# Optimization experiments

Hardware: AMD Instinct MI355X
Metric: run time of the kernel (lower is better)

Reference implementation:

```python
import jax, jax.numpy as jnp
import numpy as np

N, E, B, L = 32768, 524288, 64, 4
ESM, S, V, EH = 1280, 128, 16, 64
N_RBF = 16
CENTERS = jnp.linspace(0.0, 12.0, N_RBF)
GAMMA = 1.0 / ((12.0 / N_RBF) ** 2 + 1e-8)
LN_EPS = 1e-5


def setup_inputs() -> dict:
    key = jax.random.key(0)
    ks = iter(jax.random.split(key, 80))
    def w(shape, scale=0.02):
        return (jax.random.normal(next(ks), shape) * scale).astype(jnp.float32)
    def zeros(shape):
        return jnp.zeros(shape, jnp.float32)
    def ones(shape):
        return jnp.ones(shape, jnp.float32)
    inp = {}
    inp['x_esm'] = jax.random.normal(next(ks), (N, ESM), jnp.float32)
    inp['x_reschem'] = jax.random.normal(next(ks), (N, 6), jnp.float32)
    inp['x_role'] = jax.random.uniform(next(ks), (N, 2), jnp.float32)
    inp['x_dist_raw'] = jax.random.uniform(next(ks), (N, 4), jnp.float32) * 12.0
    inp['x_misc'] = jax.random.normal(next(ks), (N, 3), jnp.float32)
    inp['x_vec'] = jax.random.normal(next(ks), (N, 1, 3), jnp.float32)
    inp['pos'] = jax.random.normal(next(ks), (N, 3), jnp.float32) * 10.0
    inp['edge_dist_raw'] = jax.random.uniform(next(ks), (E, 2), jnp.float32) * 12.0
    # node scalar encoder
    inp['ne_esm_w'] = w((ESM, 128)); inp['ne_esm_b'] = zeros((128,))
    inp['ne_esm_ln_g'] = ones((128,)); inp['ne_esm_ln_b'] = zeros((128,))
    in_dim = 128 + 6 + 2 + 3 + 4 * N_RBF  # 203
    inp['ne_out_w'] = w((in_dim, S)); inp['ne_out_b'] = zeros((S,))
    inp['ne_out_ln_g'] = ones((S,)); inp['ne_out_ln_b'] = zeros((S,))
    # edge scalar encoder
    inp['ee_w'] = w((2 * N_RBF, EH)); inp['ee_b'] = zeros((EH,))
    inp['ee_ln_g'] = ones((EH,)); inp['ee_ln_b'] = zeros((EH,))
    inp['init_vec_w'] = w((1, V))
    # stacked per-layer params
    msi = 2 * S + EH + 1 + (2 * V + 1)  # scalar_mlp in for message gvp = 354
    usi = 2 * S + 2 * V                 # = 288
    inp['msg_s_w1'] = w((L, msi, S)); inp['msg_s_b1'] = zeros((L, S))
    inp['msg_s_w2'] = w((L, S, S)); inp['msg_s_b2'] = zeros((L, S))
    inp['msg_v_w'] = w((L, 2 * V + 1, V))
    inp['msg_g_w'] = w((L, S, V)); inp['msg_g_b'] = zeros((L, V))
    inp['upd_s_w1'] = w((L, usi, S)); inp['upd_s_b1'] = zeros((L, S))
    inp['upd_s_w2'] = w((L, S, S)); inp['upd_s_b2'] = zeros((L, S))
    inp['upd_v_w'] = w((L, 2 * V, V))
    inp['upd_g_w'] = w((L, S, V)); inp['upd_g_b'] = zeros((L, V))
    inp['ln_g'] = ones((L, S)); inp['ln_b'] = zeros((L, S))
    # heads
    inp['hm_w1'] = w((2 * S, S)); inp['hm_b1'] = zeros((S,))
    inp['hm_w2'] = w((S, 8)); inp['hm_b2'] = zeros((8,))
    inp['he_w1'] = w((2 * S, S)); inp['he_b1'] = zeros((S,))
    inp['he_w2'] = w((S, 7)); inp['he_b2'] = zeros((7,))
    inp['edge_index'] = jax.random.randint(next(ks), (2, E), 0, N, jnp.int32)
    inp['batch'] = jnp.sort(jax.random.randint(next(ks), (N,), 0, B, jnp.int32))
    return inp


def _ln(x, g, b):
    mu = x.mean(-1, keepdims=True)
    var = ((x - mu) ** 2).mean(-1, keepdims=True)
    return (x - mu) * jax.lax.rsqrt(var + LN_EPS) * g + b


def _rbf(d):
    # d [..., K] -> [..., K, N_RBF]
    return jnp.exp(-GAMMA * (d[..., None] - CENTERS) ** 2)


def _vnorm(v):
    # v [N, C, 3] -> [N, C]
    return jnp.sqrt(jnp.clip((v * v).sum(-1), 1e-8))


def _gvp(s, v, sw1, sb1, sw2, sb2, vw, gw, gb):
    s_cat = jnp.concatenate([s, _vnorm(v)], -1)
    h = jax.nn.silu(s_cat @ sw1 + sb1)
    s_out = h @ sw2 + sb2
    v_proj = jnp.einsum('nci,cv->nvi', v, vw)
    gate = jax.nn.sigmoid(s_out @ gw + gb)[..., None]
    return s_out, v_proj * gate


def _forward(x_esm, x_reschem, x_role, x_dist_raw, x_misc, x_vec, pos, edge_dist_raw,
             ne_esm_w, ne_esm_b, ne_esm_ln_g, ne_esm_ln_b, ne_out_w, ne_out_b,
             ne_out_ln_g, ne_out_ln_b, ee_w, ee_b, ee_ln_g, ee_ln_b, init_vec_w,
             msg_s_w1, msg_s_b1, msg_s_w2, msg_s_b2, msg_v_w, msg_g_w, msg_g_b,
             upd_s_w1, upd_s_b1, upd_s_w2, upd_s_b2, upd_v_w, upd_g_w, upd_g_b,
             ln_g, ln_b, hm_w1, hm_b1, hm_w2, hm_b2, he_w1, he_b1, he_w2, he_b2,
             edge_index, batch):
    n = x_esm.shape[0]
    # node scalar encoder (dropout = identity at eval)
    esm = jax.nn.silu(_ln(x_esm @ ne_esm_w + ne_esm_b, ne_esm_ln_g, ne_esm_ln_b))
    d_rbf = _rbf(x_dist_raw).reshape(n, -1)  # [N, 64]
    xcat = jnp.concatenate([esm, x_reschem, x_role, x_misc, d_rbf], -1)
    s = jax.nn.silu(_ln(xcat @ ne_out_w + ne_out_b, ne_out_ln_g, ne_out_ln_b))
    # init vector channels [N, V, 3]
    v = jnp.einsum('nci,cv->nvi', x_vec, init_vec_w)
    # edge scalar encoder
    e_rbf = _rbf(edge_dist_raw).reshape(edge_dist_raw.shape[0], -1)  # [E, 32]
    edge_s = jax.nn.silu(_ln(e_rbf @ ee_w + ee_b, ee_ln_g, ee_ln_b))
    # edge vectors [E, 1, 3]
    src, dst = edge_index[0], edge_index[1]
    rel = pos[dst] - pos[src]
    rel = rel / jnp.sqrt(jnp.clip((rel * rel).sum(-1, keepdims=True), 1e-8))
    edge_v = rel[:, None, :]
    edge_len = _vnorm(edge_v)  # [E, 1]
    for l in range(L):
        m_s_in = jnp.concatenate([s[src], s[dst], edge_s, edge_len], -1)
        m_v_in = jnp.concatenate([v[src], v[dst], edge_v], 1)
        m_s, m_v = _gvp(m_s_in, m_v_in, msg_s_w1[l], msg_s_b1[l], msg_s_w2[l],
                        msg_s_b2[l], msg_v_w[l], msg_g_w[l], msg_g_b[l])
        agg_s = jax.ops.segment_sum(m_s, dst, num_segments=n)
        agg_v = jax.ops.segment_sum(m_v, dst, num_segments=n)
        u_s_in = jnp.concatenate([s, agg_s], -1)
        u_v_in = jnp.concatenate([v, agg_v], 1)
        ds, dv = _gvp(u_s_in, u_v_in, upd_s_w1[l], upd_s_b1[l], upd_s_w2[l],
                      upd_s_b2[l], upd_v_w[l], upd_g_w[l], upd_g_b[l])
        s = _ln(s + ds, ln_g[l], ln_b[l])
        v = v + dv
    # graph pooling
    sums = jax.ops.segment_sum(s, batch, num_segments=B)
    cnts = jax.ops.segment_sum(jnp.ones((n, 1), s.dtype), batch, num_segments=B)
    pooled_mean = sums / jnp.clip(cnts, 1.0)
    pooled_max = jax.ops.segment_max(s, batch, num_segments=B)
    pooled_max = jnp.where(jnp.isfinite(pooled_max), pooled_max, 0.0)
    embed = jnp.concatenate([pooled_mean, pooled_max], -1)
    logits_metal = jax.nn.silu(embed @ hm_w1 + hm_b1) @ hm_w2 + hm_b2
    logits_ec = jax.nn.silu(embed @ he_w1 + he_b1) @ he_w2 + he_b2
    return logits_metal, logits_ec, embed


def reference(x_esm, x_reschem, x_role, x_dist_raw, x_misc, x_vec, pos, edge_dist_raw,
              ne_esm_w, ne_esm_b, ne_esm_ln_g, ne_esm_ln_b, ne_out_w, ne_out_b,
              ne_out_ln_g, ne_out_ln_b, ee_w, ee_b, ee_ln_g, ee_ln_b, init_vec_w,
              msg_s_w1, msg_s_b1, msg_s_w2, msg_s_b2, msg_v_w, msg_g_w, msg_g_b,
              upd_s_w1, upd_s_b1, upd_s_w2, upd_s_b2, upd_v_w, upd_g_w, upd_g_b,
              ln_g, ln_b, hm_w1, hm_b1, hm_w2, hm_b2, he_w1, he_b1, he_w2, he_b2,
              edge_index, batch):
    return _forward(x_esm, x_reschem, x_role, x_dist_raw, x_misc, x_vec, pos,
                    edge_dist_raw, ne_esm_w, ne_esm_b, ne_esm_ln_g, ne_esm_ln_b,
                    ne_out_w, ne_out_b, ne_out_ln_g, ne_out_ln_b, ee_w, ee_b,
                    ee_ln_g, ee_ln_b, init_vec_w, msg_s_w1, msg_s_b1, msg_s_w2,
                    msg_s_b2, msg_v_w, msg_g_w, msg_g_b, upd_s_w1, upd_s_b1,
                    upd_s_w2, upd_s_b2, upd_v_w, upd_g_w, upd_g_b, ln_g, ln_b,
                    hm_w1, hm_b1, hm_w2, hm_b2, he_w1, he_b1, he_w2, he_b2,
                    edge_index, batch)
```

## Files before the change

### kernel.cpp

```cpp
#include <hip/hip_runtime.h>
#include <hip/hip_bf16.h>
#include <cstddef>

constexpr int kN = 32768;
constexpr int kE = 524288;
constexpr int kB = 64;
constexpr int kL = 4;
constexpr float kGamma = (float)(1.0 / (0.5625 + 1e-8));
constexpr float kLnEps = 1e-5f;

#define DI __device__ __forceinline__

typedef __attribute__((ext_vector_type(8))) short bf16x8;
typedef __attribute__((ext_vector_type(4))) short s16x4;
typedef __attribute__((ext_vector_type(4))) float f32x4;
#define MFMA16(a, b, c) __builtin_amdgcn_mfma_f32_16x16x32_bf16(a, b, c, 0, 0, 0)

DI float siluf(float x) { return x / (1.f + __expf(-x)); }
DI float sigmf(float x) { return 1.f / (1.f + __expf(-x)); }
DI unsigned short f2bf(float x) {
  __hip_bfloat16 b = __float2bfloat16(x);
  return *(unsigned short*)&b;
}
DI float b2f(unsigned short u) {
  union { unsigned i; float f; } c; c.i = ((unsigned)u) << 16; return c.f;
}
DI bf16x8 ldA(const float* p) {
  const float4 a = *(const float4*)p;
  const float4 b = *(const float4*)(p + 4);
  bf16x8 r;
  r[0] = (short)f2bf(a.x); r[1] = (short)f2bf(a.y);
  r[2] = (short)f2bf(a.z); r[3] = (short)f2bf(a.w);
  r[4] = (short)f2bf(b.x); r[5] = (short)f2bf(b.y);
  r[6] = (short)f2bf(b.z); r[7] = (short)f2bf(b.w);
  return r;
}

__global__ void k_btA(const float* src, unsigned short* dst, int K) {
  int idx = blockIdx.x * 256 + threadIdx.x;
  if (idx >= K * 128) return;
  int c = idx & 127, k = idx >> 7;
  dst[c * K + k] = f2bf(src[(size_t)k * 128 + c]);
}

__global__ void k_bt1(const float* w, unsigned short* dst) {
  int idx = blockIdx.x * 256 + threadIdx.x;
  int c = idx & 127, k = idx >> 7;
  dst[c * 224 + k] = f2bf(k < 203 ? w[(size_t)k * 128 + c] : 0.f);
}

__global__ void k_btPQ(const float* w1, unsigned short* dst) {
  int idx = blockIdx.x * 256 + threadIdx.x;
  int cc = idx / 160, k = idx - cc * 160;
  int c = cc & 127, half = cc >> 7;
  float v = 0.f;
  if (k < 128) v = w1[(size_t)(half * 128 + k) * 128 + c];
  else if (k < 144) v = w1[(size_t)(321 + half * 16 + (k - 128)) * 128 + c];
  dst[idx] = f2bf(v);
}

__global__ void k_w2gw(const float* w2, const float* gw, const float* b2, const float* gb,
                       float* out) {
  int idx = blockIdx.x * 256 + threadIdx.x;
  if (idx < 2048) {
    int k = idx >> 4, t = idx & 15;
    float a = 0.f;
    for (int j = 0; j < 128; j++) a += w2[(size_t)k * 128 + j] * gw[j * 16 + t];
    out[idx] = a;
  } else if (idx < 2064) {
    int t = idx - 2048;
    float a = gb[t];
    for (int j = 0; j < 128; j++) a += b2[j] * gw[j * 16 + t];
    out[idx] = a;
  }
}

__global__ void k_xrest(const float* resch, const float* role, const float* misc,
                        const float* dist, float* xr) {
  int idx = blockIdx.x * 256 + threadIdx.x;
  int r = idx / 96, c = idx - r * 96;
  float v = 0.f;
  if (c < 6) v = resch[r * 6 + c];
  else if (c < 8) v = role[r * 2 + c - 6];
  else if (c < 11) v = misc[r * 3 + c - 8];
  else if (c < 75) {
    int j = c - 11;
    float d = dist[r * 4 + (j >> 4)];
    float t = d - 0.8f * (float)(j & 15);
    v = __expf(-kGamma * t * t);
  }
  xr[idx] = v;
}

struct G2 {
  const float* A1; const float* A2; const float* A3;
  const unsigned short* BT;
  float* out;
  unsigned short* obfP; unsigned short* obfQ;
  const float* bias; const float* lng; const float* lnb;
};

template <int MODE>
__global__ __launch_bounds__(256) void k_gemm2(G2 p) {
  constexpr int K = MODE == 0 ? 1280 : MODE == 1 ? 224 : MODE == 2 ? 160 : 288;
  constexpr int NS = K / 32;
  constexpr int NTC = (MODE == 2) ? 16 : 8;
  const int tid = threadIdx.x, lane = tid & 63, wv = tid >> 6;
  const int g4 = lane >> 4, lc = lane & 15;
  const int r = blockIdx.x * 64 + wv * 16 + lc;
  const f32x4 z = {0.f, 0.f, 0.f, 0.f};
  f32x4 acc[NTC];
#pragma unroll
  for (int nt = 0; nt < NTC; nt++) acc[nt] = z;

  if constexpr (MODE == 0) {
#pragma unroll 4
    for (int ks = 0; ks < NS; ks++) {
      const int k = ks * 32 + g4 * 8;
      const bf16x8 af = ldA(p.A1 + (size_t)r * 1280 + k);
#pragma unroll
      for (int nt = 0; nt < NTC; nt++)
        acc[nt] = MFMA16(af, *(const bf16x8*)&p.BT[(lc + 16 * nt) * K + k], acc[nt]);
    }
  } else {
#pragma unroll
    for (int ks = 0; ks < NS; ks++) {
      const int k = ks * 32 + g4 * 8;
      const float* ap;
      if constexpr (MODE == 1)
        ap = (k < 128) ? p.A1 + (size_t)r * 128 + k : p.A2 + (size_t)r * 96 + (k - 128);
      else if constexpr (MODE == 2)
        ap = (k < 128) ? p.A1 + (size_t)r * 128 + k : p.A2 + (size_t)r * 32 + (k - 128);
      else
        ap = (k < 128) ? p.A1 + (size_t)r * 128 + k
           : (k < 256) ? p.A2 + (size_t)r * 128 + (k - 128)
                       : p.A3 + (size_t)r * 32 + (k - 256);
      const bf16x8 af = ldA(ap);
#pragma unroll
      for (int nt = 0; nt < NTC; nt++)
        acc[nt] = MFMA16(af, *(const bf16x8*)&p.BT[(lc + 16 * nt) * K + k], acc[nt]);
    }
  }

  const int row0 = blockIdx.x * 64 + wv * 16 + g4 * 4;
  if constexpr (MODE == 0 || MODE == 1) {
    float bias8[8], g8[8], b8[8];
#pragma unroll
    for (int nt = 0; nt < 8; nt++) {
      int c = lc + 16 * nt;
      bias8[nt] = p.bias[c]; g8[nt] = p.lng[c]; b8[nt] = p.lnb[c];
    }
    float rsum[4] = {0.f, 0.f, 0.f, 0.f}, rsq[4] = {0.f, 0.f, 0.f, 0.f};
#pragma unroll
    for (int nt = 0; nt < 8; nt++)
#pragma unroll
      for (int i = 0; i < 4; i++) {
        float x = acc[nt][i] + bias8[nt];
        acc[nt][i] = x; rsum[i] += x; rsq[i] += x * x;
      }
#pragma unroll
    for (int m = 1; m < 16; m <<= 1)
#pragma unroll
      for (int i = 0; i < 4; i++) {
        rsum[i] += __shfl_xor(rsum[i], m);
        rsq[i] += __shfl_xor(rsq[i], m);
      }
#pragma unroll
    for (int i = 0; i < 4; i++) {
      float mu = rsum[i] * (1.f / 128.f);
      float rs = rsqrtf(rsq[i] * (1.f / 128.f) - mu * mu + kLnEps);
#pragma unroll
      for (int nt = 0; nt < 8; nt++) {
        float y = (acc[nt][i] - mu) * rs * g8[nt] + b8[nt];
        p.out[(size_t)(row0 + i) * 128 + lc + 16 * nt] = siluf(y);
      }
    }
  } else if constexpr (MODE == 2) {
#pragma unroll
    for (int i = 0; i < 4; i++) {
      bf16x8 po, qo;
#pragma unroll
      for (int nt = 0; nt < 8; nt++) {
        po[nt] = (short)f2bf(acc[nt][i]);
        qo[nt] = (short)f2bf(acc[nt + 8][i] + p.bias[lc + 16 * nt]);
      }
      *(bf16x8*)&p.obfP[(size_t)(row0 + i) * 128 + lc * 8] = po;
      *(bf16x8*)&p.obfQ[(size_t)(row0 + i) * 128 + lc * 8] = qo;
    }
  } else {
#pragma unroll
    for (int nt = 0; nt < 8; nt++) {
      float bv = p.bias[lc + 16 * nt];
#pragma unroll
      for (int i = 0; i < 4; i++)
        p.out[(size_t)(row0 + i) * 128 + lc + 16 * nt] = siluf(acc[nt][i] + bv);
    }
  }
}

__global__ void k_v0(const float* xv, const float* ivw, float* v) {
  int idx = blockIdx.x * 256 + threadIdx.x;
  int n = idx / 48, f = idx % 48, t = f / 3, i = f - t * 3;
  v[idx] = xv[n * 3 + i] * ivw[t];
}

__global__ void k_vn(const float* v, float* vn) {
  int idx = blockIdx.x * 256 + threadIdx.x;
  int n = idx >> 5, t = idx & 31;
  float val = 0.f;
  if (t < 16) {
    const float* b = &v[(size_t)n * 48 + t * 3];
    val = sqrtf(fmaxf(b[0] * b[0] + b[1] * b[1] + b[2] * b[2], 1e-8f));
  }
  vn[idx] = val;
}

__global__ void k_vab(const float* v, const float* vw,
                      unsigned short* VAb, unsigned short* VBb) {
  int idx = blockIdx.x * 256 + threadIdx.x;
  int n = idx >> 4, t = idx & 15;
  float a0 = 0.f, a1 = 0.f, a2 = 0.f, b0 = 0.f, b1 = 0.f, b2 = 0.f;
#pragma unroll
  for (int c = 0; c < 16; c++) {
    float wa = vw[c * 16 + t], wb = vw[(16 + c) * 16 + t];
    float x0 = v[(size_t)n * 48 + c * 3 + 0];
    float x1 = v[(size_t)n * 48 + c * 3 + 1];
    float x2 = v[(size_t)n * 48 + c * 3 + 2];
    a0 += x0 * wa; a1 += x1 * wa; a2 += x2 * wa;
    b0 += x0 * wb; b1 += x1 * wb; b2 += x2 * wb;
  }
  s16x4 A, Bv;
  A[0] = (short)f2bf(a0); A[1] = (short)f2bf(a1); A[2] = (short)f2bf(a2); A[3] = 0;
  Bv[0] = (short)f2bf(b0); Bv[1] = (short)f2bf(b1); Bv[2] = (short)f2bf(b2); Bv[3] = 0;
  *(s16x4*)&VAb[(size_t)n * 64 + t * 4] = A;
  *(s16x4*)&VBb[(size_t)n * 64 + t * 4] = Bv;
}

__global__ void k_hist(const int* ei, int* cnt) {
  int e = blockIdx.x * 256 + threadIdx.x;
  atomicAdd(&cnt[ei[kE + e]], 1);
}

__global__ __launch_bounds__(1024) void k_scan(const int* cnt, int* rowstart, int* cursor) {
  __shared__ int part[1024];
  const int t = threadIdx.x;
  const int base = t * 32;
  int loc[32];
  int s = 0;
#pragma unroll
  for (int i = 0; i < 32; i++) { loc[i] = cnt[base + i]; s += loc[i]; }
  part[t] = s;
  __syncthreads();
  for (int off = 1; off < 1024; off <<= 1) {
    int val = (t >= off) ? part[t - off] : 0;
    __syncthreads();
    part[t] += val;
    __syncthreads();
  }
  int run = (t == 0) ? 0 : part[t - 1];
#pragma unroll
  for (int i = 0; i < 32; i++) {
    rowstart[base + i] = run;
    cursor[base + i] = run;
    run += loc[i];
  }
  if (t == 1023) rowstart[kN] = run;
}

__global__ void k_scatter(const int* ei, const float* pos, int* cursor,
                          int* prm, int* srcp, float* relp, float* lenp) {
  int e = blockIdx.x * 256 + threadIdx.x;
  int a = ei[e], b = ei[kE + e];
  int p = atomicAdd(&cursor[b], 1);
  prm[p] = e;
  srcp[p] = a;
  float dx = pos[(size_t)b * 3 + 0] - pos[(size_t)a * 3 + 0];
  float dy = pos[(size_t)b * 3 + 1] - pos[(size_t)a * 3 + 1];
  float dz = pos[(size_t)b * 3 + 2] - pos[(size_t)a * 3 + 2];
  float n2 = dx * dx + dy * dy + dz * dz;
  float inv = 1.f / sqrtf(fmaxf(n2, 1e-8f));
  float rx = dx * inv, ry = dy * inv, rz = dz * inv;
  relp[(size_t)p * 3 + 0] = rx; relp[(size_t)p * 3 + 1] = ry; relp[(size_t)p * 3 + 2] = rz;
  lenp[p] = sqrtf(fmaxf(rx * rx + ry * ry + rz * rz, 1e-8f));
}

__global__ __launch_bounds__(256) void k_enc_mfma(
    const int* __restrict__ prm, const float* __restrict__ edr,
    const float* __restrict__ eew, const float* __restrict__ eeb,
    const float* __restrict__ lg, const float* __restrict__ lb,
    __hip_bfloat16* __restrict__ enc) {
  __shared__ unsigned short eewT[64 * 32];
  const int tid = threadIdx.x;
#pragma unroll
  for (int i = 0; i < 8; i++) {
    int idx = tid + i * 256;
    int col = idx >> 5, k = idx & 31;
    eewT[col * 32 + k] = f2bf(eew[k * 64 + col]);
  }
  __syncthreads();

  const int lane = tid & 63, wv = tid >> 6;
  const int g4 = lane >> 4, lc = lane & 15;
  const int e0 = blockIdx.x * 64 + wv * 16;

  const int e = prm[e0 + lc];
  const float d = edr[(size_t)e * 2 + (g4 >> 1)];
  const float c0 = 0.8f * (float)((g4 & 1) * 8);
  bf16x8 af;
#pragma unroll
  for (int j = 0; j < 8; j++) {
    float t = d - (c0 + 0.8f * (float)j);
    af[j] = (short)f2bf(__expf(-kGamma * t * t));
  }
  const f32x4 z = {0.f, 0.f, 0.f, 0.f};
  f32x4 acc[4];
#pragma unroll
  for (int ct = 0; ct < 4; ct++)
    acc[ct] = MFMA16(af, *(const bf16x8*)&eewT[(ct * 16 + lc) * 32 + g4 * 8], z);

  float bias4[4], g4v[4], b4[4];
#pragma unroll
  for (int ct = 0; ct < 4; ct++) {
    int col = ct * 16 + lc;
    bias4[ct] = eeb[col]; g4v[ct] = lg[col]; b4[ct] = lb[col];
  }
  float rsum[4] = {0.f, 0.f, 0.f, 0.f}, rsq[4] = {0.f, 0.f, 0.f, 0.f};
#pragma unroll
  for (int ct = 0; ct < 4; ct++)
#pragma unroll
    for (int i = 0; i < 4; i++) {
      float x = acc[ct][i] + bias4[ct];
      acc[ct][i] = x; rsum[i] += x; rsq[i] += x * x;
    }
#pragma unroll
  for (int m = 1; m < 16; m <<= 1)
#pragma unroll
    for (int i = 0; i < 4; i++) {
      rsum[i] += __shfl_xor(rsum[i], m);
      rsq[i] += __shfl_xor(rsq[i], m);
    }
#pragma unroll
  for (int i = 0; i < 4; i++) {
    float mu = rsum[i] * (1.f / 64.f);
    float rs = rsqrtf(rsq[i] * (1.f / 64.f) - mu * mu + kLnEps);
    const size_t row = (size_t)(e0 + g4 * 4 + i);
#pragma unroll
    for (int ct = 0; ct < 4; ct++) {
      float y = (acc[ct][i] - mu) * rs * g4v[ct] + b4[ct];
      enc[row * 64 + ct * 16 + lc] = __float2bfloat16(siluf(y));
    }
  }
}

struct __align__(16) EMS2 {
  unsigned short we1T[128 * 72];
  unsigned short w2T[128 * 136];
  unsigned short w2gwT[16 * 72];
  unsigned short h[8][16 * 72];
  float wlen[128];
  float b2[128];
  float gb[16];
  float vw32[16];
};

__global__ __launch_bounds__(512, 4) void k_node_msg(
    const unsigned short* __restrict__ Pb, const unsigned short* __restrict__ Qb,
    const unsigned short* __restrict__ VAb, const unsigned short* __restrict__ VBb,
    const __hip_bfloat16* __restrict__ enc_, const float* __restrict__ relp,
    const float* __restrict__ lenp, const int* __restrict__ srcp,
    const int* __restrict__ rowstart, const float* __restrict__ vglob,
    const float* __restrict__ w1, const float* __restrict__ w2g,
    const float* __restrict__ b2g, const float* __restrict__ w2gw,
    const float* __restrict__ vwg,
    float* __restrict__ aggs, float* __restrict__ aggv, float* __restrict__ vnu) {
  __shared__ EMS2 sm;
  const int tid = threadIdx.x;
  const unsigned short* enc = (const unsigned short*)enc_;

#pragma unroll
  for (int i = 0; i < 16; i++) {
    int idx = tid + i * 512; int k = idx >> 7, n = idx & 127;
    sm.we1T[n * 72 + k] = f2bf(w1[(size_t)(256 + k) * 128 + n]);
  }
#pragma unroll
  for (int i = 0; i < 32; i++) {
    int idx = tid + i * 512; int k = idx >> 7, n = idx & 127;
    sm.w2T[n * 136 + k] = f2bf(w2g[(size_t)k * 128 + n]);
  }
#pragma unroll
  for (int i = 0; i < 4; i++) {
    int idx = tid + i * 512; int k = idx >> 4, t = idx & 15;
    sm.w2gwT[t * 72 + k] = f2bf(w2gw[k * 16 + t]);
  }
  if (tid < 128) { sm.wlen[tid] = w1[320 * 128 + tid] + w1[353 * 128 + tid]; sm.b2[tid] = b2g[tid]; }
  if (tid < 16) { sm.gb[tid] = w2gw[2048 + tid]; sm.vw32[tid] = vwg[512 + tid]; }
  __syncthreads();

  const int lane = tid & 63, wv = tid >> 6;
  const int g4 = lane >> 4;
  const int lc = lane & 15;
  unsigned short* hrow = &sm.h[wv][0];

  float wlenR[8], b2R[8];
#pragma unroll
  for (int nt = 0; nt < 8; nt++) { wlenR[nt] = sm.wlen[lc + 16 * nt]; b2R[nt] = sm.b2[lc + 16 * nt]; }
  const float gbR = sm.gb[lc];
  const float vwR = sm.vw32[lc];
  const f32x4 z = {0.f, 0.f, 0.f, 0.f};

  for (int n = blockIdx.x * 8 + wv; n < kN; n += gridDim.x * 8) {
    const int r0 = rowstart[n], r1 = rowstart[n + 1];
    float qR[8], vbR[3];
    {
      const bf16x8 qv = *(const bf16x8*)&Qb[(size_t)n * 128 + lc * 8];
#pragma unroll
      for (int nt = 0; nt < 8; nt++) qR[nt] = b2f((unsigned short)qv[nt]);
      const s16x4 vbv = *(const s16x4*)&VBb[(size_t)n * 64 + lc * 4];
#pragma unroll
      for (int j = 0; j < 3; j++) vbR[j] = b2f((unsigned short)vbv[j]);
    }
    float colsum[8];
#pragma unroll
    for (int nt = 0; nt < 8; nt++) colsum[nt] = 0.f;
    float av0 = 0.f, av1 = 0.f, av2 = 0.f;

    for (int base = r0; base < r1; base += 16) {
      int nv = r1 - base; if (nv > 16) nv = 16;

      int pa = base + lc; if (pa >= kE) pa = kE - 1;
      const bf16x8 a0 = *(const bf16x8*)&enc[(size_t)pa * 64 + g4 * 8];
      const bf16x8 a1 = *(const bf16x8*)&enc[(size_t)pa * 64 + 32 + g4 * 8];
      f32x4 acc[8];
#pragma unroll
      for (int nt = 0; nt < 8; nt++) {
        acc[nt] = MFMA16(a0, *(const bf16x8*)&sm.we1T[(lc + 16 * nt) * 72 + g4 * 8], z);
        acc[nt] = MFMA16(a1, *(const bf16x8*)&sm.we1T[(lc + 16 * nt) * 72 + 32 + g4 * 8], acc[nt]);
      }

      int sn[4], pr[4]; float le[4];
#pragma unroll
      for (int i = 0; i < 4; i++) {
        int p = base + g4 * 4 + i; if (p >= kE) p = kE - 1;
        pr[i] = p; sn[i] = srcp[p]; le[i] = lenp[p];
      }
#pragma unroll
      for (int i = 0; i < 4; i++) {
        const bf16x8 pbv = *(const bf16x8*)&Pb[(size_t)sn[i] * 128 + lc * 8];
#pragma unroll
        for (int nt = 0; nt < 8; nt++)
          acc[nt][i] += b2f((unsigned short)pbv[nt]) + qR[nt] + le[i] * wlenR[nt];
      }

      f32x4 m[8]; f32x4 gac;
#pragma unroll
      for (int i = 0; i < 4; i++)
#pragma unroll
        for (int nt = 0; nt < 4; nt++)
          hrow[(g4 * 4 + i) * 72 + lc + 16 * nt] = f2bf(siluf(acc[nt][i]));
      {
        const bf16x8 aB0 = *(const bf16x8*)&hrow[lc * 72 + g4 * 8];
        const bf16x8 aB1 = *(const bf16x8*)&hrow[lc * 72 + 32 + g4 * 8];
#pragma unroll
        for (int nt = 0; nt < 8; nt++) {
          m[nt] = MFMA16(aB0, *(const bf16x8*)&sm.w2T[(lc + 16 * nt) * 136 + g4 * 8], z);
          m[nt] = MFMA16(aB1, *(const bf16x8*)&sm.w2T[(lc + 16 * nt) * 136 + 32 + g4 * 8], m[nt]);
        }
        gac = MFMA16(aB0, *(const bf16x8*)&sm.w2gwT[lc * 72 + g4 * 8], z);
        gac = MFMA16(aB1, *(const bf16x8*)&sm.w2gwT[lc * 72 + 32 + g4 * 8], gac);
      }
#pragma unroll
      for (int i = 0; i < 4; i++)
#pragma unroll
        for (int nt = 4; nt < 8; nt++)
          hrow[(g4 * 4 + i) * 72 + lc + 16 * (nt - 4)] = f2bf(siluf(acc[nt][i]));
      {
        const bf16x8 aB2 = *(const bf16x8*)&hrow[lc * 72 + g4 * 8];
        const bf16x8 aB3 = *(const bf16x8*)&hrow[lc * 72 + 32 + g4 * 8];
#pragma unroll
        for (int nt = 0; nt < 8; nt++) {
          m[nt] = MFMA16(aB2, *(const bf16x8*)&sm.w2T[(lc + 16 * nt) * 136 + 64 + g4 * 8], m[nt]);
          m[nt] = MFMA16(aB3, *(const bf16x8*)&sm.w2T[(lc + 16 * nt) * 136 + 96 + g4 * 8], m[nt]);
        }
        gac = MFMA16(aB2, *(const bf16x8*)&sm.w2gwT[lc * 72 + 64 + g4 * 8], gac);
        gac = MFMA16(aB3, *(const bf16x8*)&sm.w2gwT[lc * 72 + 96 + g4 * 8], gac);
      }
#pragma unroll
      for (int nt = 0; nt < 8; nt++) {
#pragma unroll
        for (int i = 0; i < 4; i++) m[nt][i] += b2R[nt];
      }

#pragma unroll
      for (int i = 0; i < 4; i++) {
        const int row = g4 * 4 + i;
        if (row < nv) {
#pragma unroll
          for (int nt = 0; nt < 8; nt++) colsum[nt] += m[nt][i];
          float g = sigmf(gac[i] + gbR);
          const s16x4 vav = *(const s16x4*)&VAb[(size_t)sn[i] * 64 + lc * 4];
          const float* rp = &relp[(size_t)pr[i] * 3];
          av0 += g * (b2f((unsigned short)vav[0]) + vbR[0] + rp[0] * vwR);
          av1 += g * (b2f((unsigned short)vav[1]) + vbR[1] + rp[1] * vwR);
          av2 += g * (b2f((unsigned short)vav[2]) + vbR[2] + rp[2] * vwR);
        }
      }
    }

#pragma unroll
    for (int nt = 0; nt < 8; nt++) {
      colsum[nt] += __shfl_xor(colsum[nt], 16);
      colsum[nt] += __shfl_xor(colsum[nt], 32);
    }
    av0 += __shfl_xor(av0, 16); av0 += __shfl_xor(av0, 32);
    av1 += __shfl_xor(av1, 16); av1 += __shfl_xor(av1, 32);
    av2 += __shfl_xor(av2, 16); av2 += __shfl_xor(av2, 32);

    if (g4 == 0) {
#pragma unroll
      for (int nt = 0; nt < 8; nt++) aggs[(size_t)n * 128 + lc + 16 * nt] = colsum[nt];
      aggv[(size_t)n * 48 + lc * 3 + 0] = av0;
      aggv[(size_t)n * 48 + lc * 3 + 1] = av1;
      aggv[(size_t)n * 48 + lc * 3 + 2] = av2;
      vnu[(size_t)n * 32 + 16 + lc] = sqrtf(fmaxf(av0 * av0 + av1 * av1 + av2 * av2, 1e-8f));
    } else if (g4 == 1) {
      float x0 = vglob[(size_t)n * 48 + lc * 3 + 0];
      float x1 = vglob[(size_t)n * 48 + lc * 3 + 1];
      float x2 = vglob[(size_t)n * 48 + lc * 3 + 2];
      vnu[(size_t)n * 32 + lc] = sqrtf(fmaxf(x0 * x0 + x1 * x1 + x2 * x2, 1e-8f));
    }
  }
}

__global__ __launch_bounds__(256) void k_upd2(
    const float* __restrict__ hupd, const unsigned short* __restrict__ BuT,
    const float* __restrict__ b2,
    const float* __restrict__ ugw, const float* __restrict__ ugb, const float* __restrict__ uvw,
    const float* __restrict__ aggv, const float* __restrict__ lng, const float* __restrict__ lnb,
    float* __restrict__ s, float* __restrict__ v, float* __restrict__ vnout) {
  __shared__ __align__(16) float dsb[64 * 129];
  __shared__ float smu[64], srs[64];
  __shared__ float uvwS[512];
  const int tid = threadIdx.x;
  const int bm = blockIdx.x * 64;
  const int lane = tid & 63, wv = tid >> 6;
  const int g4 = lane >> 4, lc = lane & 15;
  uvwS[tid] = uvw[tid]; uvwS[tid + 256] = uvw[tid + 256];
  const f32x4 z = {0.f, 0.f, 0.f, 0.f};
  const int r = bm + wv * 16 + lc;
  f32x4 acc[8];
#pragma unroll
  for (int nt = 0; nt < 8; nt++) acc[nt] = z;

#pragma unroll
  for (int ks = 0; ks < 4; ks++) {
    const int k = ks * 32 + g4 * 8;
    const bf16x8 af = ldA(hupd + (size_t)r * 128 + k);
#pragma unroll
    for (int nt = 0; nt < 8; nt++)
      acc[nt] = MFMA16(af, *(const bf16x8*)&BuT[(lc + 16 * nt) * 128 + k], acc[nt]);
  }
#pragma unroll
  for (int nt = 0; nt < 8; nt++) {
    float bv = b2[lc + 16 * nt];
#pragma unroll
    for (int i = 0; i < 4; i++)
      dsb[(wv * 16 + g4 * 4 + i) * 129 + lc + 16 * nt] = acc[nt][i] + bv;
  }
  __syncthreads();

  const int rr = tid >> 2, p = tid & 3;
  const int n = bm + rr;
  float g[4];
#pragma unroll
  for (int j = 0; j < 4; j++) g[j] = ugb[p * 4 + j];
#pragma unroll 8
  for (int k = 0; k < 128; k++) {
    float m = dsb[rr * 129 + k];
    const float4 wg = *(const float4*)&ugw[k * 16 + p * 4];
    g[0] += m * wg.x; g[1] += m * wg.y; g[2] += m * wg.z; g[3] += m * wg.w;
  }
#pragma unroll
  for (int j = 0; j < 4; j++) g[j] = sigmf(g[j]);

  float vnew[12];
#pragma unroll
  for (int i2 = 0; i2 < 3; i2++) {
    float xv[16], xa[16];
#pragma unroll
    for (int c = 0; c < 16; c++) {
      xv[c] = v[(size_t)n * 48 + c * 3 + i2];
      xa[c] = aggv[(size_t)n * 48 + c * 3 + i2];
    }
#pragma unroll
    for (int j = 0; j < 4; j++) {
      int t = p * 4 + j;
      float a = 0.f;
#pragma unroll
      for (int c = 0; c < 16; c++)
        a += xv[c] * uvwS[c * 16 + t] + xa[c] * uvwS[(16 + c) * 16 + t];
      vnew[j * 3 + i2] = xv[t] + a * g[j];
    }
  }
  if (tid < 64) {
    float sm = 0.f, sq = 0.f;
    for (int c = 0; c < 128; c++) {
      float x = s[(size_t)(bm + tid) * 128 + c] + dsb[tid * 129 + c];
      sm += x; sq += x * x;
    }
    float mu = sm * (1.f / 128.f);
    float var = sq * (1.f / 128.f) - mu * mu;
    smu[tid] = mu; srs[tid] = rsqrtf(var + kLnEps);
  }
  __syncthreads();
#pragma unroll
  for (int j = 0; j < 4; j++) {
    float n0 = vnew[j * 3 + 0], n1 = vnew[j * 3 + 1], n2 = vnew[j * 3 + 2];
#pragma unroll
    for (int i2 = 0; i2 < 3; i2++)
      v[(size_t)n * 48 + (p * 4 + j) * 3 + i2] = vnew[j * 3 + i2];
    vnout[(size_t)n * 32 + p * 4 + j] = sqrtf(fmaxf(n0 * n0 + n1 * n1 + n2 * n2, 1e-8f));
    vnout[(size_t)n * 32 + 16 + p * 4 + j] = 0.f;
  }
#pragma unroll 4
  for (int i = 0; i < 32; i++) {
    int idx = tid + i * 256; int rw = idx >> 7, c = idx & 127;
    float x = s[(size_t)(bm + rw) * 128 + c] + dsb[rw * 129 + c];
    float y = (x - smu[rw]) * srs[rw] * lng[c] + lnb[c];
    s[(size_t)(bm + rw) * 128 + c] = y;
  }
}

DI int lbound(const int* b, int nn, int key) {
  int lo = 0, hi = nn;
  while (lo < hi) { int m = (lo + hi) >> 1; if (b[m] < key) lo = m + 1; else hi = m; }
  return lo;
}

__global__ void k_pool(const float* s, const int* batch, float* dout) {
  int g = blockIdx.x, tid = threadIdx.x;
  int lo = lbound(batch, kN, g), hi = lbound(batch, kN, g + 1);
  float sum = 0.f, mx = -3.402823e38f;
  for (int n = lo; n < hi; n++) {
    float x = s[(size_t)n * 128 + tid];
    sum += x; mx = fmaxf(mx, x);
  }
  int cnt = hi - lo;
  float mean = sum / fmaxf((float)cnt, 1.f);
  if (cnt == 0) mx = 0.f;
  dout[960 + g * 256 + tid] = mean;
  dout[960 + g * 256 + 128 + tid] = mx;
}

__global__ void k_heads(const float* hw1, const float* hb1, const float* hw2, const float* hb2,
                        const float* ew1, const float* eb1, const float* ew2, const float* eb2,
                        float* dout) {
  __shared__ float emb[256], h1[256];
  int g = blockIdx.x, tid = threadIdx.x;
  emb[tid] = dout[960 + g * 256 + tid];
  emb[128 + tid] = dout[960 + g * 256 + 128 + tid];
  __syncthreads();
  float am = hb1[tid], ae = eb1[tid];
#pragma unroll 4
  for (int k = 0; k < 256; k++) {
    float e = emb[k];
    am += e * hw1[k * 128 + tid];
    ae += e * ew1[k * 128 + tid];
  }
  h1[tid] = siluf(am); h1[128 + tid] = siluf(ae);
  __syncthreads();
  if (tid < 8) {
    float a = hb2[tid];
    for (int j = 0; j < 128; j++) a += h1[j] * hw2[j * 8 + tid];
    dout[g * 8 + tid] = a;
  } else if (tid >= 64 && tid < 71) {
    int o = tid - 64;
    float a = eb2[o];
    for (int j = 0; j < 128; j++) a += h1[128 + j] * ew2[j * 7 + o];
    dout[512 + g * 7 + o] = a;
  }
}

extern "C" void kernel_launch(void* const* d_in, const int* in_sizes, int n_in,
                              void* d_out, int out_size, void* d_ws, size_t ws_size,
                              hipStream_t stream) {
  (void)in_sizes; (void)n_in; (void)out_size; (void)ws_size;
  const float* x_esm   = (const float*)d_in[0];
  const float* x_resch = (const float*)d_in[1];
  const float* x_role  = (const float*)d_in[2];
  const float* x_dist  = (const float*)d_in[3];
  const float* x_misc  = (const float*)d_in[4];
  const float* x_vec   = (const float*)d_in[5];
  const float* pos     = (const float*)d_in[6];
  const float* edr     = (const float*)d_in[7];
  const float* ne_esm_w = (const float*)d_in[8];
  const float* ne_esm_b = (const float*)d_in[9];
  const float* ne_esm_lg = (const float*)d_in[10];
  const float* ne_esm_lb = (const float*)d_in[11];
  const float* ne_out_w = (const float*)d_in[12];
  const float* ne_out_b = (const float*)d_in[13];
  const float* ne_out_lg = (const float*)d_in[14];
  const float* ne_out_lb = (const float*)d_in[15];
  const float* ee_w = (const float*)d_in[16];
  const float* ee_b = (const float*)d_in[17];
  const float* ee_lg = (const float*)d_in[18];
  const float* ee_lb = (const float*)d_in[19];
  const float* ivw = (const float*)d_in[20];
  const float* msg_w1 = (const float*)d_in[21];
  const float* msg_b1 = (const float*)d_in[22];
  const float* msg_w2 = (const float*)d_in[23];
  const float* msg_b2 = (const float*)d_in[24];
  const float* msg_vw = (const float*)d_in[25];
  const float* msg_gw = (const float*)d_in[26];
  const float* msg_gb = (const float*)d_in[27];
  const float* upd_w1 = (const float*)d_in[28];
  const float* upd_b1 = (const float*)d_in[29];
  const float* upd_w2 = (const float*)d_in[30];
  const float* upd_b2 = (const float*)d_in[31];
  const float* upd_vw = (const float*)d_in[32];
  const float* upd_gw = (const float*)d_in[33];
  const float* upd_gb = (const float*)d_in[34];
  const float* ln_g = (const float*)d_in[35];
  const float* ln_b = (const float*)d_in[36];
  const float* hm_w1 = (const float*)d_in[37];
  const float* hm_b1 = (const float*)d_in[38];
  const float* hm_w2 = (const float*)d_in[39];
  const float* hm_b2 = (const float*)d_in[40];
  const float* he_w1 = (const float*)d_in[41];
  const float* he_b1 = (const float*)d_in[42];
  const float* he_w2 = (const float*)d_in[43];
  const float* he_b2 = (const float*)d_in[44];
  const int* ei = (const int*)d_in[45];
  const int* batch = (const int*)d_in[46];
  float* dout = (float*)d_out;

  size_t off = 0;
  auto alloc = [&](size_t bytes) {
    void* p = (char*)d_ws + off;
    off += (bytes + 255) & ~(size_t)255;
    return p;
  };
  float* s    = (float*)alloc((size_t)kN * 128 * 4);
  float* v    = (float*)alloc((size_t)kN * 48 * 4);
  float* vn   = (float*)alloc((size_t)kN * 32 * 4);
  unsigned short* Pb = (unsigned short*)alloc((size_t)kN * 128 * 2);
  unsigned short* Qb = (unsigned short*)alloc((size_t)kN * 128 * 2);
  unsigned short* VAb = (unsigned short*)alloc((size_t)kN * 64 * 2);
  unsigned short* VBb = (unsigned short*)alloc((size_t)kN * 64 * 2);
  float* aggS = (float*)alloc((size_t)kN * 128 * 4);
  float* aggV = (float*)alloc((size_t)kN * 48 * 4);
  float* vnu  = (float*)alloc((size_t)kN * 32 * 4);
  float* hupd = (float*)alloc((size_t)kN * 128 * 4);
  float* xrest = (float*)alloc((size_t)kN * 96 * 4);
  __hip_bfloat16* enc = (__hip_bfloat16*)alloc((size_t)kE * 64 * 2);
  float* relp = (float*)alloc((size_t)kE * 3 * 4);
  float* lenp = (float*)alloc((size_t)kE * 4);
  int* srcp   = (int*)alloc((size_t)kE * 4);
  int* prm    = (int*)alloc((size_t)kE * 4);
  int* cnt    = (int*)alloc((size_t)kN * 4);
  int* rowstart = (int*)alloc((size_t)(kN + 1) * 4);
  int* cursor = (int*)alloc((size_t)kN * 4);
  unsigned short* B0T = (unsigned short*)alloc((size_t)128 * 1280 * 2);
  unsigned short* B1T = (unsigned short*)alloc((size_t)128 * 224 * 2);
  unsigned short* B23T = (unsigned short*)alloc((size_t)kL * 256 * 160 * 2);
  unsigned short* B4T = (unsigned short*)alloc((size_t)kL * 128 * 288 * 2);
  unsigned short* BuT = (unsigned short*)alloc((size_t)kL * 128 * 128 * 2);
  float* w2gwL = (float*)alloc((size_t)kL * 2064 * 4);
  float* esm = hupd;

  hipMemsetAsync(cnt, 0, (size_t)kN * 4, stream);
  k_hist<<<kE / 256, 256, 0, stream>>>(ei, cnt);
  k_scan<<<1, 1024, 0, stream>>>(cnt, rowstart, cursor);
  k_scatter<<<kE / 256, 256, 0, stream>>>(ei, pos, cursor, prm, srcp, relp, lenp);
  k_enc_mfma<<<kE / 64, 256, 0, stream>>>(prm, edr, ee_w, ee_b, ee_lg, ee_lb, enc);
  k_btA<<<(1280 * 128 + 255) / 256, 256, 0, stream>>>(ne_esm_w, B0T, 1280);
  k_bt1<<<(224 * 128 + 255) / 256, 256, 0, stream>>>(ne_out_w, B1T);
  k_xrest<<<(kN * 96 + 255) / 256, 256, 0, stream>>>(x_resch, x_role, x_misc, x_dist, xrest);
  for (int l = 0; l < kL; l++) {
    k_btPQ<<<(256 * 160 + 255) / 256, 256, 0, stream>>>(msg_w1 + (size_t)l * 354 * 128,
                                                        B23T + (size_t)l * 256 * 160);
    k_btA<<<(288 * 128 + 255) / 256, 256, 0, stream>>>(upd_w1 + (size_t)l * 288 * 128,
                                                       B4T + (size_t)l * 128 * 288, 288);
    k_btA<<<(128 * 128 + 255) / 256, 256, 0, stream>>>(upd_w2 + (size_t)l * 128 * 128,
                                                       BuT + (size_t)l * 128 * 128, 128);
    k_w2gw<<<9, 256, 0, stream>>>(msg_w2 + (size_t)l * 128 * 128, msg_gw + l * 128 * 16,
                                  msg_b2 + l * 128, msg_gb + l * 16, w2gwL + (size_t)l * 2064);
  }

  {
    G2 p{}; p.A1 = x_esm; p.BT = B0T; p.out = esm;
    p.bias = ne_esm_b; p.lng = ne_esm_lg; p.lnb = ne_esm_lb;
    k_gemm2<0><<<kN / 64, 256, 0, stream>>>(p);
  }
  {
    G2 p{}; p.A1 = esm; p.A2 = xrest; p.BT = B1T; p.out = s;
    p.bias = ne_out_b; p.lng = ne_out_lg; p.lnb = ne_out_lb;
    k_gemm2<1><<<kN / 64, 256, 0, stream>>>(p);
  }
  k_v0<<<kN * 48 / 256, 256, 0, stream>>>(x_vec, ivw, v);
  k_vn<<<kN * 32 / 256, 256, 0, stream>>>(v, vn);

  for (int l = 0; l < kL; l++) {
    const float* w1l = msg_w1 + (size_t)l * 354 * 128;
    const float* b1l = msg_b1 + l * 128;
    const float* w2l = msg_w2 + (size_t)l * 128 * 128;
    const float* b2l = msg_b2 + l * 128;
    const float* vwl = msg_vw + l * 33 * 16;
    const float* ub1 = upd_b1 + l * 128;
    const float* ub2 = upd_b2 + l * 128;
    const float* uvwl = upd_vw + l * 32 * 16;
    const float* ugwl = upd_gw + l * 128 * 16;
    const float* ugbl = upd_gb + l * 16;
    const float* lgl = ln_g + l * 128;
    const float* lbl = ln_b + l * 128;

    {
      G2 p{}; p.A1 = s; p.A2 = vn; p.BT = B23T + (size_t)l * 256 * 160;
      p.obfP = Pb; p.obfQ = Qb; p.bias = b1l;
      k_gemm2<2><<<kN / 64, 256, 0, stream>>>(p);
    }
    k_vab<<<kN * 16 / 256, 256, 0, stream>>>(v, vwl, VAb, VBb);
    k_node_msg<<<512, 512, 0, stream>>>(Pb, Qb, VAb, VBb, enc, relp, lenp, srcp,
                                        rowstart, v, w1l, w2l, b2l,
                                        w2gwL + (size_t)l * 2064, vwl,
                                        aggS, aggV, vnu);
    {
      G2 p{}; p.A1 = s; p.A2 = aggS; p.A3 = vnu; p.BT = B4T + (size_t)l * 128 * 288;
      p.out = hupd; p.bias = ub1;
      k_gemm2<4><<<kN / 64, 256, 0, stream>>>(p);
    }
    k_upd2<<<kN / 64, 256, 0, stream>>>(hupd, BuT + (size_t)l * 128 * 128, ub2,
                                        ugwl, ugbl, uvwl, aggV, lgl, lbl, s, v, vn);
  }

  k_pool<<<kB, 128, 0, stream>>>(s, batch, dout);
  k_heads<<<kB, 128, 0, stream>>>(hm_w1, hm_b1, hm_w2, hm_b2,
                                  he_w1, he_b1, he_w2, he_b2, dout);
}
```

Before: 1.747 ms.

## Fold edge-length and Q terms into MFMA, transpose message layout, stage P/Q stores through LDS

Result: slower. 1.857 ms (+6.3%).

```diff
diff --git a/kernel.cpp b/kernel.cpp
--- a/kernel.cpp
+++ b/kernel.cpp
@@ -176,16 +176,34 @@
       }
     }
   } else if constexpr (MODE == 2) {
-#pragma unroll
-    for (int i = 0; i < 4; i++) {
-      bf16x8 po, qo;
-#pragma unroll
-      for (int nt = 0; nt < 8; nt++) {
-        po[nt] = (short)f2bf(acc[nt][i]);
-        qo[nt] = (short)f2bf(acc[nt + 8][i] + p.bias[lc + 16 * nt]);
-      }
-      *(bf16x8*)&p.obfP[(size_t)(row0 + i) * 128 + lc * 8] = po;
-      *(bf16x8*)&p.obfQ[(size_t)(row0 + i) * 128 + lc * 8] = qo;
+    __shared__ unsigned short sb[64 * 136];
+    const int rl = tid >> 2, seg = tid & 3;
+#pragma unroll
+    for (int nt = 0; nt < 8; nt++)
+#pragma unroll
+      for (int i = 0; i < 4; i++)
+        sb[(wv * 16 + g4 * 4 + i) * 136 + lc + 16 * nt] = f2bf(acc[nt][i]);
+    __syncthreads();
+    {
+      size_t gr = (size_t)(blockIdx.x * 64 + rl) * 128 + seg * 32;
+#pragma unroll
+      for (int u = 0; u < 4; u++)
+        *(bf16x8*)&p.obfP[gr + u * 8] = *(const bf16x8*)&sb[rl * 136 + seg * 32 + u * 8];
+    }
+    __syncthreads();
+#pragma unroll
+    for (int nt = 0; nt < 8; nt++) {
+      float bv = p.bias[lc + 16 * nt];
+#pragma unroll
+      for (int i = 0; i < 4; i++)
+        sb[(wv * 16 + g4 * 4 + i) * 136 + lc + 16 * nt] = f2bf(acc[nt + 8][i] + bv);
+    }
+    __syncthreads();
+    {
+      size_t gr = (size_t)(blockIdx.x * 64 + rl) * 128 + seg * 32;
+#pragma unroll
+      for (int u = 0; u < 4; u++)
+        *(bf16x8*)&p.obfQ[gr + u * 8] = *(const bf16x8*)&sb[rl * 136 + seg * 32 + u * 8];
     }
   } else {
 #pragma unroll
@@ -352,12 +370,12 @@
   }
 }
 
-struct __align__(16) EMS2 {
+struct __align__(16) EMS3 {
   unsigned short we1T[128 * 72];
   unsigned short w2T[128 * 136];
   unsigned short w2gwT[16 * 72];
   unsigned short h[8][16 * 72];
-  float wlen[128];
+  unsigned short Aext[8][256];
   float b2[128];
   float gb[16];
   float vw32[16];
@@ -373,7 +391,7 @@
     const float* __restrict__ b2g, const float* __restrict__ w2gw,
     const float* __restrict__ vwg,
     float* __restrict__ aggs, float* __restrict__ aggv, float* __restrict__ vnu) {
-  __shared__ EMS2 sm;
+  __shared__ EMS3 sm;
   const int tid = threadIdx.x;
   const unsigned short* enc = (const unsigned short*)enc_;
 
@@ -392,7 +410,12 @@
     int idx = tid + i * 512; int k = idx >> 4, t = idx & 15;
     sm.w2gwT[t * 72 + k] = f2bf(w2gw[k * 16 + t]);
   }
-  if (tid < 128) { sm.wlen[tid] = w1[320 * 128 + tid] + w1[353 * 128 + tid]; sm.b2[tid] = b2g[tid]; }
+#pragma unroll
+  for (int i = 0; i < 2; i++) {
+    int idx = tid + i * 512; int w = idx >> 7, oc = idx & 127;
+    sm.Aext[w][oc * 2] = f2bf(w1[320 * 128 + oc] + w1[353 * 128 + oc]);
+  }
+  if (tid < 128) sm.b2[tid] = b2g[tid];
   if (tid < 16) { sm.gb[tid] = w2gw[2048 + tid]; sm.vw32[tid] = vwg[512 + tid]; }
   __syncthreads();
 
@@ -400,21 +423,24 @@
   const int g4 = lane >> 4;
   const int lc = lane & 15;
   unsigned short* hrow = &sm.h[wv][0];
-
-  float wlenR[8], b2R[8];
-#pragma unroll
-  for (int nt = 0; nt < 8; nt++) { wlenR[nt] = sm.wlen[lc + 16 * nt]; b2R[nt] = sm.b2[lc + 16 * nt]; }
+  unsigned short* aext = &sm.Aext[wv][0];
+
+  float b2R[8];
+#pragma unroll
+  for (int nt = 0; nt < 8; nt++) b2R[nt] = sm.b2[lc + 16 * nt];
   const float gbR = sm.gb[lc];
   const float vwR = sm.vw32[lc];
   const f32x4 z = {0.f, 0.f, 0.f, 0.f};
 
   for (int n = blockIdx.x * 8 + wv; n < kN; n += gridDim.x * 8) {
     const int r0 = rowstart[n], r1 = rowstart[n + 1];
-    float qR[8], vbR[3];
     {
-      const bf16x8 qv = *(const bf16x8*)&Qb[(size_t)n * 128 + lc * 8];
-#pragma unroll
-      for (int nt = 0; nt < 8; nt++) qR[nt] = b2f((unsigned short)qv[nt]);
+      unsigned qv = *(const unsigned*)&Qb[(size_t)n * 128 + lane * 2];
+      aext[lane * 4 + 1] = (unsigned short)(qv & 0xffffu);
+      aext[lane * 4 + 3] = (unsigned short)(qv >> 16);
+    }
+    float vbR[3];
+    {
       const s16x4 vbv = *(const s16x4*)&VBb[(size_t)n * 64 + lc * 4];
 #pragma unroll
       for (int j = 0; j < 3; j++) vbR[j] = b2f((unsigned short)vbv[j]);
@@ -428,77 +454,69 @@
       int nv = r1 - base; if (nv > 16) nv = 16;
 
       int pa = base + lc; if (pa >= kE) pa = kE - 1;
+      const int psrc = srcp[pa];
+      const float le = lenp[pa];
       const bf16x8 a0 = *(const bf16x8*)&enc[(size_t)pa * 64 + g4 * 8];
       const bf16x8 a1 = *(const bf16x8*)&enc[(size_t)pa * 64 + 32 + g4 * 8];
-      f32x4 acc[8];
-#pragma unroll
-      for (int nt = 0; nt < 8; nt++) {
-        acc[nt] = MFMA16(a0, *(const bf16x8*)&sm.we1T[(lc + 16 * nt) * 72 + g4 * 8], z);
-        acc[nt] = MFMA16(a1, *(const bf16x8*)&sm.we1T[(lc + 16 * nt) * 72 + 32 + g4 * 8], acc[nt]);
-      }
-
-      int sn[4], pr[4]; float le[4];
-#pragma unroll
-      for (int i = 0; i < 4; i++) {
-        int p = base + g4 * 4 + i; if (p >= kE) p = kE - 1;
-        pr[i] = p; sn[i] = srcp[p]; le[i] = lenp[p];
-      }
-#pragma unroll
-      for (int i = 0; i < 4; i++) {
-        const bf16x8 pbv = *(const bf16x8*)&Pb[(size_t)sn[i] * 128 + lc * 8];
-#pragma unroll
-        for (int nt = 0; nt < 8; nt++)
-          acc[nt][i] += b2f((unsigned short)pbv[nt]) + qR[nt] + le[i] * wlenR[nt];
-      }
-
-      f32x4 m[8]; f32x4 gac;
-#pragma unroll
-      for (int i = 0; i < 4; i++)
-#pragma unroll
-        for (int nt = 0; nt < 4; nt++)
-          hrow[(g4 * 4 + i) * 72 + lc + 16 * nt] = f2bf(siluf(acc[nt][i]));
-      {
-        const bf16x8 aB0 = *(const bf16x8*)&hrow[lc * 72 + g4 * 8];
-        const bf16x8 aB1 = *(const bf16x8*)&hrow[lc * 72 + 32 + g4 * 8];
-#pragma unroll
-        for (int nt = 0; nt < 8; nt++) {
-          m[nt] = MFMA16(aB0, *(const bf16x8*)&sm.w2T[(lc + 16 * nt) * 136 + g4 * 8], z);
-          m[nt] = MFMA16(aB1, *(const bf16x8*)&sm.w2T[(lc + 16 * nt) * 136 + 32 + g4 * 8], m[nt]);
+      bf16x8 be = {0, 0, 0, 0, 0, 0, 0, 0};
+      if (g4 == 0) { be[0] = (short)f2bf(le); be[1] = (short)0x3F80; }
+
+      f32x4 m[8];
+#pragma unroll
+      for (int nt = 0; nt < 8; nt++) m[nt] = z;
+      f32x4 gac = z;
+
+#pragma unroll
+      for (int hh = 0; hh < 2; hh++) {
+        f32x4 acc[4];
+#pragma unroll
+        for (int q = 0; q < 4; q++) {
+          const int nt = hh * 4 + q;
+          const bf16x8 wA0 = *(const bf16x8*)&sm.we1T[(nt * 16 + lc) * 72 + g4 * 8];
+          const bf16x8 wA1 = *(const bf16x8*)&sm.we1T[(nt * 16 + lc) * 72 + 32 + g4 * 8];
+          acc[q] = MFMA16(wA0, a0, z);
+          acc[q] = MFMA16(wA1, a1, acc[q]);
+          bf16x8 ax = {0, 0, 0, 0, 0, 0, 0, 0};
+          if (g4 == 0) {
+            unsigned u = *(const unsigned*)&aext[(nt * 16 + lc) * 2];
+            ax[0] = (short)(u & 0xffffu); ax[1] = (short)(u >> 16);
+          }
+          acc[q] = MFMA16(ax, be, acc[q]);
         }
-        gac = MFMA16(aB0, *(const bf16x8*)&sm.w2gwT[lc * 72 + g4 * 8], z);
-        gac = MFMA16(aB1, *(const bf16x8*)&sm.w2gwT[lc * 72 + 32 + g4 * 8], gac);
-      }
-#pragma unroll
-      for (int i = 0; i < 4; i++)
-#pragma unroll
-        for (int nt = 4; nt < 8; nt++)
-          hrow[(g4 * 4 + i) * 72 + lc + 16 * (nt - 4)] = f2bf(siluf(acc[nt][i]));
-      {
-        const bf16x8 aB2 = *(const bf16x8*)&hrow[lc * 72 + g4 * 8];
-        const bf16x8 aB3 = *(const bf16x8*)&hrow[lc * 72 + 32 + g4 * 8];
-#pragma unroll
-        for (int nt = 0; nt < 8; nt++) {
-          m[nt] = MFMA16(aB2, *(const bf16x8*)&sm.w2T[(lc + 16 * nt) * 136 + 64 + g4 * 8], m[nt]);
-          m[nt] = MFMA16(aB3, *(const bf16x8*)&sm.w2T[(lc + 16 * nt) * 136 + 96 + g4 * 8], m[nt]);
+#pragma unroll
+        for (int q = 0; q < 4; q++) {
+          const int nt = hh * 4 + q;
+          const s16x4 pv = *(const s16x4*)&Pb[(size_t)psrc * 128 + nt * 16 + g4 * 4];
+          s16x4 hv;
+#pragma unroll
+          for (int i = 0; i < 4; i++)
+            hv[i] = (short)f2bf(siluf(acc[q][i] + b2f((unsigned short)pv[i])));
+          *(s16x4*)&hrow[lc * 72 + q * 16 + g4 * 4] = hv;
         }
-        gac = MFMA16(aB2, *(const bf16x8*)&sm.w2gwT[lc * 72 + 64 + g4 * 8], gac);
-        gac = MFMA16(aB3, *(const bf16x8*)&sm.w2gwT[lc * 72 + 96 + g4 * 8], gac);
-      }
-#pragma unroll
-      for (int nt = 0; nt < 8; nt++) {
-#pragma unroll
-        for (int i = 0; i < 4; i++) m[nt][i] += b2R[nt];
+        {
+          const bf16x8 aB0 = *(const bf16x8*)&hrow[lc * 72 + g4 * 8];
+          const bf16x8 aB1 = *(const bf16x8*)&hrow[lc * 72 + 32 + g4 * 8];
+#pragma unroll
+          for (int nt2 = 0; nt2 < 8; nt2++) {
+            m[nt2] = MFMA16(aB0, *(const bf16x8*)&sm.w2T[(lc + 16 * nt2) * 136 + hh * 64 + g4 * 8], m[nt2]);
+            m[nt2] = MFMA16(aB1, *(const bf16x8*)&sm.w2T[(lc + 16 * nt2) * 136 + hh * 64 + 32 + g4 * 8], m[nt2]);
+          }
+          gac = MFMA16(aB0, *(const bf16x8*)&sm.w2gwT[lc * 72 + hh * 64 + g4 * 8], gac);
+          gac = MFMA16(aB1, *(const bf16x8*)&sm.w2gwT[lc * 72 + hh * 64 + 32 + g4 * 8], gac);
+        }
       }
 
 #pragma unroll
       for (int i = 0; i < 4; i++) {
         const int row = g4 * 4 + i;
         if (row < nv) {
-#pragma unroll
-          for (int nt = 0; nt < 8; nt++) colsum[nt] += m[nt][i];
+          int p2 = base + row;
+#pragma unroll
+          for (int nt = 0; nt < 8; nt++) colsum[nt] += m[nt][i] + b2R[nt];
           float g = sigmf(gac[i] + gbR);
-          const s16x4 vav = *(const s16x4*)&VAb[(size_t)sn[i] * 64 + lc * 4];
-          const float* rp = &relp[(size_t)pr[i] * 3];
+          const int sn2 = srcp[p2];
+          const s16x4 vav = *(const s16x4*)&VAb[(size_t)sn2 * 64 + lc * 4];
+          const float* rp = &relp[(size_t)p2 * 3];
           av0 += g * (b2f((unsigned short)vav[0]) + vbR[0] + rp[0] * vwR);
           av1 += g * (b2f((unsigned short)vav[1]) + vbR[1] + rp[1] * vwR);
           av2 += g * (b2f((unsigned short)vav[2]) + vbR[2] + rp[2] * vwR);
```

## Fuse update-MLP first GEMM into update kernel via LDS bf16 staging

Applied to the files above, without the earlier changes.

Result: faster. 1.669 ms (-4.5%).

```diff
diff --git a/kernel.cpp b/kernel.cpp
--- a/kernel.cpp
+++ b/kernel.cpp
@@ -102,7 +102,7 @@
 
 template <int MODE>
 __global__ __launch_bounds__(256) void k_gemm2(G2 p) {
-  constexpr int K = MODE == 0 ? 1280 : MODE == 1 ? 224 : MODE == 2 ? 160 : 288;
+  constexpr int K = MODE == 0 ? 1280 : MODE == 1 ? 224 : 160;
   constexpr int NS = K / 32;
   constexpr int NTC = (MODE == 2) ? 16 : 8;
   const int tid = threadIdx.x, lane = tid & 63, wv = tid >> 6;
@@ -129,12 +129,8 @@
       const float* ap;
       if constexpr (MODE == 1)
         ap = (k < 128) ? p.A1 + (size_t)r * 128 + k : p.A2 + (size_t)r * 96 + (k - 128);
-      else if constexpr (MODE == 2)
+      else
         ap = (k < 128) ? p.A1 + (size_t)r * 128 + k : p.A2 + (size_t)r * 32 + (k - 128);
-      else
-        ap = (k < 128) ? p.A1 + (size_t)r * 128 + k
-           : (k < 256) ? p.A2 + (size_t)r * 128 + (k - 128)
-                       : p.A3 + (size_t)r * 32 + (k - 256);
       const bf16x8 af = ldA(ap);
 #pragma unroll
       for (int nt = 0; nt < NTC; nt++)
@@ -175,7 +171,7 @@
         p.out[(size_t)(row0 + i) * 128 + lc + 16 * nt] = siluf(y);
       }
     }
-  } else if constexpr (MODE == 2) {
+  } else {
 #pragma unroll
     for (int i = 0; i < 4; i++) {
       bf16x8 po, qo;
@@ -186,14 +182,6 @@
       }
       *(bf16x8*)&p.obfP[(size_t)(row0 + i) * 128 + lc * 8] = po;
       *(bf16x8*)&p.obfQ[(size_t)(row0 + i) * 128 + lc * 8] = qo;
-    }
-  } else {
-#pragma unroll
-    for (int nt = 0; nt < 8; nt++) {
-      float bv = p.bias[lc + 16 * nt];
-#pragma unroll
-      for (int i = 0; i < 4; i++)
-        p.out[(size_t)(row0 + i) * 128 + lc + 16 * nt] = siluf(acc[nt][i] + bv);
     }
   }
 }
@@ -531,13 +519,16 @@
   }
 }
 
-__global__ __launch_bounds__(256) void k_upd2(
-    const float* __restrict__ hupd, const unsigned short* __restrict__ BuT,
+__global__ __launch_bounds__(256) void k_upd_fused(
+    const float* __restrict__ sA, const float* __restrict__ aggS,
+    const float* __restrict__ vnu, const unsigned short* __restrict__ B4T,
+    const float* __restrict__ ub1, const unsigned short* __restrict__ BuT,
     const float* __restrict__ b2,
     const float* __restrict__ ugw, const float* __restrict__ ugb, const float* __restrict__ uvw,
     const float* __restrict__ aggv, const float* __restrict__ lng, const float* __restrict__ lnb,
     float* __restrict__ s, float* __restrict__ v, float* __restrict__ vnout) {
   __shared__ __align__(16) float dsb[64 * 129];
+  __shared__ __align__(16) unsigned short hb[64 * 136];
   __shared__ float smu[64], srs[64];
   __shared__ float uvwS[512];
   const int tid = threadIdx.x;
@@ -547,24 +538,47 @@
   uvwS[tid] = uvw[tid]; uvwS[tid + 256] = uvw[tid + 256];
   const f32x4 z = {0.f, 0.f, 0.f, 0.f};
   const int r = bm + wv * 16 + lc;
+
   f32x4 acc[8];
 #pragma unroll
   for (int nt = 0; nt < 8; nt++) acc[nt] = z;
-
+#pragma unroll
+  for (int ks = 0; ks < 9; ks++) {
+    const int k = ks * 32 + g4 * 8;
+    const float* ap = (k < 128) ? sA + (size_t)r * 128 + k
+                    : (k < 256) ? aggS + (size_t)r * 128 + (k - 128)
+                                : vnu + (size_t)r * 32 + (k - 256);
+    const bf16x8 af = ldA(ap);
+#pragma unroll
+    for (int nt = 0; nt < 8; nt++)
+      acc[nt] = MFMA16(af, *(const bf16x8*)&B4T[(lc + 16 * nt) * 288 + k], acc[nt]);
+  }
+#pragma unroll
+  for (int nt = 0; nt < 8; nt++) {
+    float bv = ub1[lc + 16 * nt];
+#pragma unroll
+    for (int i = 0; i < 4; i++)
+      hb[(wv * 16 + g4 * 4 + i) * 136 + lc + 16 * nt] = f2bf(siluf(acc[nt][i] + bv));
+  }
+  __syncthreads();
+
+  f32x4 acc2[8];
+#pragma unroll
+  for (int nt = 0; nt < 8; nt++) acc2[nt] = z;
 #pragma unroll
   for (int ks = 0; ks < 4; ks++) {
     const int k = ks * 32 + g4 * 8;
-    const bf16x8 af = ldA(hupd + (size_t)r * 128 + k);
+    const bf16x8 af = *(const bf16x8*)&hb[(wv * 16 + lc) * 136 + k];
 #pragma unroll
     for (int nt = 0; nt < 8; nt++)
-      acc[nt] = MFMA16(af, *(const bf16x8*)&BuT[(lc + 16 * nt) * 128 + k], acc[nt]);
+      acc2[nt] = MFMA16(af, *(const bf16x8*)&BuT[(lc + 16 * nt) * 128 + k], acc2[nt]);
   }
 #pragma unroll
   for (int nt = 0; nt < 8; nt++) {
     float bv = b2[lc + 16 * nt];
 #pragma unroll
     for (int i = 0; i < 4; i++)
-      dsb[(wv * 16 + g4 * 4 + i) * 129 + lc + 16 * nt] = acc[nt][i] + bv;
+      dsb[(wv * 16 + g4 * 4 + i) * 129 + lc + 16 * nt] = acc2[nt][i] + bv;
   }
   __syncthreads();
 
@@ -823,13 +837,10 @@
                                         rowstart, v, w1l, w2l, b2l,
                                         w2gwL + (size_t)l * 2064, vwl,
                                         aggS, aggV, vnu);
-    {
-      G2 p{}; p.A1 = s; p.A2 = aggS; p.A3 = vnu; p.BT = B4T + (size_t)l * 128 * 288;
-      p.out = hupd; p.bias = ub1;
-      k_gemm2<4><<<kN / 64, 256, 0, stream>>>(p);
-    }
-    k_upd2<<<kN / 64, 256, 0, stream>>>(hupd, BuT + (size_t)l * 128 * 128, ub2,
-                                        ugwl, ugbl, uvwl, aggV, lgl, lbl, s, v, vn);
+    k_upd_fused<<<kN / 64, 256, 0, stream>>>(s, aggS, vnu,
+                                             B4T + (size_t)l * 128 * 288, ub1,
+                                             BuT + (size_t)l * 128 * 128, ub2,
+                                             ugwl, ugbl, uvwl, aggV, lgl, lbl, s, v, vn);
   }
 
   k_pool<<<kB, 128, 0, stream>>>(s, batch, dout);
```
